# Optimization experiments

Hardware: AMD Instinct MI355X
Metric: run time of the kernel (lower is better)

## Reference

```python
import jax, jax.numpy as jnp
import numpy as np

B, N, C, H = 2, 2048, 1024, 16
D = C // H  # head dim = 64
EPS = 1e-12  # torch F.normalize eps


def l2norm(t):
    # F.normalize(t, dim=-1): x / max(||x||_2, eps)
    n = jnp.linalg.norm(t, axis=-1, keepdims=True)
    return t / jnp.maximum(n, EPS)


def setup_inputs() -> dict:
    key = jax.random.key(0)
    k1, k2, k3 = jax.random.split(key, 3)
    x = jax.random.normal(k1, (B, N, C), dtype=jnp.float32)
    qkv_w = jax.random.normal(k2, (3 * C, C), dtype=jnp.float32) * (1.0 / np.sqrt(C))
    temperature = jnp.ones((H, 1, 1), dtype=jnp.float32)
    proj_w = jax.random.normal(k3, (C, C), dtype=jnp.float32) * (1.0 / np.sqrt(C))
    proj_b = jnp.zeros((C,), dtype=jnp.float32)
    return {"x": x, "qkv_w": qkv_w, "temperature": temperature,
            "proj_w": proj_w, "proj_b": proj_b}


def reference(x, qkv_w, temperature, proj_w, proj_b):
    b, n, c = x.shape
    qkv = jnp.einsum('bnc,fc->bnf', x, qkv_w)           # [B,N,3C], no bias
    q, k, v = jnp.split(qkv, 3, axis=-1)                # each [B,N,C]
    # l2-normalize over FULL channel dim (before head split), as in source
    q = l2norm(q)
    k = l2norm(k)
    # split heads -> [B,H,N,D]
    q = q.reshape(b, n, H, D).transpose(0, 2, 1, 3)
    k = k.reshape(b, n, H, D).transpose(0, 2, 1, 3)
    v = v.reshape(b, n, H, D).transpose(0, 2, 1, 3)
    scale = 1.0 / np.sqrt(D)
    q = q * scale
    k = k * scale
    attn = jnp.einsum('bhnd,bhkd->bhnk', q, k)          # [B,H,N,N]
    attn = attn / temperature                           # (H,1,1) broadcasts
    attn = jax.nn.softmax(attn, axis=-1)
    out = jnp.einsum('bhnk,bhkd->bhnd', attn, v)        # [B,H,N,D]
    out = out.transpose(0, 2, 1, 3).reshape(b, n, c)    # [B,N,C]
    out = jnp.einsum('bnc,oc->bno', out, proj_w) + proj_b
    return out
```

## Files before the change

### kernel.cpp

```cpp
#include <hip/hip_runtime.h>

typedef __bf16 bf16;
using bf16x2 = __attribute__((ext_vector_type(2))) bf16;
using bf16x4 = __attribute__((ext_vector_type(4))) bf16;
using bf16x8 = __attribute__((ext_vector_type(8))) bf16;
using f32x4  = __attribute__((ext_vector_type(4))) float;

#define DEVI __device__ __forceinline__

DEVI void gload_lds16(const void* g, void* l) {
  __builtin_amdgcn_global_load_lds((const __attribute__((address_space(1))) void*)g,
                                   (__attribute__((address_space(3))) void*)l, 16, 0, 0);
}

DEVI float exp2_fast(float x) { return __builtin_amdgcn_exp2f(x); }

__global__ __launch_bounds__(256) void k_cvt3(
    const float* __restrict__ a, bf16* __restrict__ oa,
    const float* __restrict__ b, bf16* __restrict__ ob,
    const float* __restrict__ c, bf16* __restrict__ oc) {
  const int blk = blockIdx.x;
  const float* in; bf16* out; int i;
  if (blk < 4096)      { in = a; out = oa; i = blk * 256 + threadIdx.x; }
  else if (blk < 7168) { in = b; out = ob; i = (blk - 4096) * 256 + threadIdx.x; }
  else                 { in = c; out = oc; i = (blk - 7168) * 256 + threadIdx.x; }
  f32x4 v = ((const f32x4*)in)[i];
  bf16x4 o = {(bf16)v.x, (bf16)v.y, (bf16)v.z, (bf16)v.w};
  ((bf16x4*)out)[i] = o;
}

template<int OUT_BF16, int HAS_BIAS>
__global__ __launch_bounds__(256) void k_gemm_bt(
    const bf16* __restrict__ A, const bf16* __restrict__ W,
    const float* __restrict__ bias, void* __restrict__ outp,
    int Kk, int Nout)
{
  __shared__ __align__(16) bf16 As[128 * 32];
  __shared__ __align__(16) bf16 Bs[128 * 32];
  const int t = threadIdx.x;
  const int lane = t & 63, wv = t >> 6;
  const int l15 = lane & 15, l4 = lane >> 4;
  const int nbx = gridDim.x;
  const int fb = blockIdx.y * nbx + blockIdx.x;
  const int cpx = (nbx * gridDim.y) >> 3;
  const int swz = (fb & 7) * cpx + (fb >> 3);
  const int row0 = (swz % nbx) * 128, col0 = (swz / nbx) * 128;
  const int wr = wv >> 1, wc = wv & 1;

  f32x4 acc[4][4];
  #pragma unroll
  for (int m = 0; m < 4; ++m)
    #pragma unroll
    for (int n = 0; n < 4; ++n) acc[m][n] = (f32x4){0.f, 0.f, 0.f, 0.f};

  const int g0 = t, g1 = t + 256;
  const bf16* ga0 = A + (size_t)(row0 + (g0 >> 2)) * Kk + (g0 & 3) * 8;
  const bf16* ga1 = A + (size_t)(row0 + (g1 >> 2)) * Kk + (g1 & 3) * 8;
  const bf16* gb0 = W + (size_t)(col0 + (g0 >> 2)) * Kk + (g0 & 3) * 8;
  const bf16* gb1 = W + (size_t)(col0 + (g1 >> 2)) * Kk + (g1 & 3) * 8;
  char* la0 = (char*)As + wv * 1024;
  char* la1 = (char*)As + 4096 + wv * 1024;
  char* lb0 = (char*)Bs + wv * 1024;
  char* lb1 = (char*)Bs + 4096 + wv * 1024;

  const int nk = Kk >> 5;
  for (int kt = 0; kt < nk; ++kt) {
    __syncthreads();
    gload_lds16(ga0 + kt * 32, la0);
    gload_lds16(ga1 + kt * 32, la1);
    gload_lds16(gb0 + kt * 32, lb0);
    gload_lds16(gb1 + kt * 32, lb1);
    __syncthreads();
    bf16x8 af[4], bfv[4];
    #pragma unroll
    for (int m = 0; m < 4; ++m)
      af[m] = *(const bf16x8*)(As + (wr * 64 + m * 16 + l15) * 32 + l4 * 8);
    #pragma unroll
    for (int n = 0; n < 4; ++n)
      bfv[n] = *(const bf16x8*)(Bs + (wc * 64 + n * 16 + l15) * 32 + l4 * 8);
    #pragma unroll
    for (int m = 0; m < 4; ++m)
      #pragma unroll
      for (int n = 0; n < 4; ++n)
        acc[m][n] = __builtin_amdgcn_mfma_f32_16x16x32_bf16(af[m], bfv[n], acc[m][n], 0, 0, 0);
  }

  #pragma unroll
  for (int n = 0; n < 4; ++n) {
    const int col = col0 + wc * 64 + n * 16 + l15;
    float bv = HAS_BIAS ? bias[col] : 0.f;
    #pragma unroll
    for (int m = 0; m < 4; ++m) {
      #pragma unroll
      for (int r = 0; r < 4; ++r) {
        const int row = row0 + wr * 64 + m * 16 + l4 * 4 + r;
        float v = acc[m][n][r] + bv;
        if (OUT_BF16) ((bf16*)outp)[(size_t)row * Nout + col] = (bf16)v;
        else          ((float*)outp)[(size_t)row * Nout + col] = v;
      }
    }
  }
}

__global__ __launch_bounds__(256) void k_rownorm(const bf16* __restrict__ qkv,
                                                 float* __restrict__ invq,
                                                 float* __restrict__ invk)
{
  const int row = blockIdx.x * 4 + (threadIdx.x >> 6);
  const int lane = threadIdx.x & 63;
  const bf16* p = qkv + (size_t)row * 3072 + lane * 16;
  float sq = 0.f, sk = 0.f;
  bf16x8 a0 = *(const bf16x8*)(p);
  bf16x8 a1 = *(const bf16x8*)(p + 8);
  bf16x8 b0 = *(const bf16x8*)(p + 1024);
  bf16x8 b1 = *(const bf16x8*)(p + 1032);
  #pragma unroll
  for (int j = 0; j < 8; ++j) {
    float x0 = (float)a0[j], x1 = (float)a1[j];
    float y0 = (float)b0[j], y1 = (float)b1[j];
    sq += x0 * x0 + x1 * x1;
    sk += y0 * y0 + y1 * y1;
  }
  #pragma unroll
  for (int m = 1; m <= 32; m <<= 1) {
    sq += __shfl_xor(sq, m);
    sk += __shfl_xor(sk, m);
  }
  if (lane == 0) {
    invq[row] = 0.125f / fmaxf(sqrtf(sq), 1e-12f);
    invk[row] = 0.125f / fmaxf(sqrtf(sk), 1e-12f);
  }
}

__global__ __launch_bounds__(256) void k_scatter(
    const bf16* __restrict__ qkv, const float* __restrict__ invq,
    const float* __restrict__ invk, const float* __restrict__ temperature,
    bf16* __restrict__ Qh, bf16* __restrict__ Kh, bf16* __restrict__ Vt)
{
  __shared__ __align__(16) bf16 vt[64][72];
  const int t = threadIdx.x;
  const int b = blockIdx.z, h = blockIdx.y;
  const int n0 = blockIdx.x * 64;
  const float tfac = 1.4426950408889634f / temperature[h];
  {
    const int nl = t >> 2;
    const int d0 = (t & 3) << 4;
    const size_t row = (size_t)b * 2048 + n0 + nl;
    const bf16* src = qkv + row * 3072 + h * 64 + d0;
    const float fq = invq[row];
    const float fk = invk[row] * tfac;
    bf16x8 q0 = *(const bf16x8*)(src);
    bf16x8 q1 = *(const bf16x8*)(src + 8);
    bf16x8 k0 = *(const bf16x8*)(src + 1024);
    bf16x8 k1 = *(const bf16x8*)(src + 1032);
    bf16x8 v0 = *(const bf16x8*)(src + 2048);
    bf16x8 v1 = *(const bf16x8*)(src + 2056);
    bf16x8 qo, ko;
    #pragma unroll
    for (int j = 0; j < 8; ++j) {
      qo[j] = (bf16)((float)q0[j] * fq);
      ko[j] = (bf16)((float)k0[j] * fk);
    }
    size_t orow = ((size_t)(b * 16 + h) * 2048 + n0 + nl) * 64 + d0;
    *(bf16x8*)(Qh + orow) = qo;
    *(bf16x8*)(Kh + orow) = ko;
    #pragma unroll
    for (int j = 0; j < 8; ++j) {
      qo[j] = (bf16)((float)q1[j] * fq);
      ko[j] = (bf16)((float)k1[j] * fk);
    }
    *(bf16x8*)(Qh + orow + 8) = qo;
    *(bf16x8*)(Kh + orow + 8) = ko;
    *(bf16x8*)&vt[nl][d0] = v0;
    *(bf16x8*)&vt[nl][d0 + 8] = v1;
  }
  __syncthreads();
  {
    const int d = t >> 2;
    const int nc = (t & 3) << 4;
    bf16x8 o0, o1;
    #pragma unroll
    for (int j = 0; j < 8; ++j) { o0[j] = vt[nc + j][d]; o1[j] = vt[nc + 8 + j][d]; }
    size_t obase = ((size_t)(b * 16 + h) * 64 + d) * 2048 + n0 + nc;
    *(bf16x8*)(Vt + obase) = o0;
    *(bf16x8*)(Vt + obase + 8) = o1;
  }
}

__global__ __launch_bounds__(512, 4) void k_attn(
    const bf16* __restrict__ Qh, const bf16* __restrict__ Kh,
    const bf16* __restrict__ Vt, bf16* __restrict__ ao)
{
  __shared__ __align__(16) bf16 Kb[2][64 * 64];
  __shared__ __align__(16) bf16 Vb[2][64 * 64];
  __shared__ __align__(16) bf16 Pl[8][16 * 64];
  const int t = threadIdx.x, lane = t & 63, wv = t >> 6;
  const int l15 = lane & 15, l4 = lane >> 4;

  const int bid = blockIdx.x;
  const int swz = (bid & 7) * 64 + (bid >> 3);
  const int plane_id = swz >> 4;
  const int qb = swz & 15;
  const int b = plane_id >> 4, h = plane_id & 15;
  const int q0 = qb * 128 + wv * 16;

  const size_t plane = (size_t)plane_id * (2048 * 64);
  const bf16* Qp = Qh + plane;
  const bf16* Kp = Kh + plane;
  const bf16* Vp = Vt + plane;

  const int srow = t >> 3;
  const int sc = (t & 7) ^ (srow & 7);
  const bf16* gK = Kp + (size_t)srow * 64 + sc * 8;
  const bf16* gV = Vp + (size_t)srow * 2048 + sc * 8;
  char* lK0 = (char*)&Kb[0][0] + wv * 1024;
  char* lK1 = (char*)&Kb[1][0] + wv * 1024;
  char* lV0 = (char*)&Vb[0][0] + wv * 1024;
  char* lV1 = (char*)&Vb[1][0] + wv * 1024;

  bf16x8 qf0 = *(const bf16x8*)(Qp + (q0 + l15) * 64 + l4 * 8);
  bf16x8 qf1 = *(const bf16x8*)(Qp + (q0 + l15) * 64 + 32 + l4 * 8);

  bf16x8 vones;
  #pragma unroll
  for (int j = 0; j < 8; ++j) vones[j] = (bf16)1.0f;

  f32x4 accO[4];
  #pragma unroll
  for (int df = 0; df < 4; ++df) accO[df] = (f32x4){0.f, 0.f, 0.f, 0.f};
  f32x4 accS = (f32x4){0.f, 0.f, 0.f, 0.f};

  bf16* pw = &Pl[wv][0] + l15 * 64;
  const int pxor = (l15 & 7) << 3;

#define STAGE(bi, kv0_)                                           \
  do {                                                            \
    gload_lds16(gK + (size_t)(kv0_) * 64, (bi) ? lK1 : lK0);      \
    gload_lds16(gV + (kv0_),              (bi) ? lV1 : lV0);      \
  } while (0)

  STAGE(0, 0);
  __syncthreads();

  int cur = 0;
  for (int kt = 0; kt < 32; ++kt) {
    if (kt < 31) STAGE(cur ^ 1, (kt + 1) * 64);

    const bf16* kb = &Kb[cur][0];
    const bf16* vb = &Vb[cur][0];

    f32x4 s[4];
    __builtin_amdgcn_s_setprio(1);
    #pragma unroll
    for (int kvf = 0; kvf < 4; ++kvf) {
      const int row = kvf * 16 + l15;
      const int r7 = row & 7;
      bf16x8 kf0 = *(const bf16x8*)(kb + row * 64 + ((l4 ^ r7) * 8));
      bf16x8 kf1 = *(const bf16x8*)(kb + row * 64 + (((4 + l4) ^ r7) * 8));
      s[kvf] = (f32x4){0.f, 0.f, 0.f, 0.f};
      s[kvf] = __builtin_amdgcn_mfma_f32_16x16x32_bf16(kf0, qf0, s[kvf], 0, 0, 0);
      s[kvf] = __builtin_amdgcn_mfma_f32_16x16x32_bf16(kf1, qf1, s[kvf], 0, 0, 0);
    }
    __builtin_amdgcn_s_setprio(0);
    #pragma unroll
    for (int kvf = 0; kvf < 4; ++kvf)
      #pragma unroll
      for (int rp = 0; rp < 2; ++rp) {
        bf16x2 pv = {(bf16)exp2_fast(s[kvf][2 * rp]),
                     (bf16)exp2_fast(s[kvf][2 * rp + 1])};
        *(bf16x2*)(pw + ((kvf * 16 + l4 * 4 + 2 * rp) ^ pxor)) = pv;
      }
    __builtin_amdgcn_s_setprio(1);
    #pragma unroll
    for (int ss = 0; ss < 2; ++ss) {
      bf16x8 pf = *(const bf16x8*)(pw + (((ss * 32 + l4 * 8)) ^ pxor));
      accS = __builtin_amdgcn_mfma_f32_16x16x32_bf16(pf, vones, accS, 0, 0, 0);
      #pragma unroll
      for (int df = 0; df < 4; ++df) {
        const int row = df * 16 + l15;
        bf16x8 vf = *(const bf16x8*)(vb + row * 64 + (((ss * 4 + l4) ^ (row & 7)) * 8));
        accO[df] = __builtin_amdgcn_mfma_f32_16x16x32_bf16(pf, vf, accO[df], 0, 0, 0);
      }
    }
    __builtin_amdgcn_s_setprio(0);
    __syncthreads();
    cur ^= 1;
  }
#undef STAGE

  #pragma unroll
  for (int r = 0; r < 4; ++r) {
    const float inv = 1.f / accS[r];
    const size_t orow = ((size_t)b * 2048 + q0 + l4 * 4 + r) * 1024 + h * 64;
    #pragma unroll
    for (int df = 0; df < 4; ++df)
      ao[orow + df * 16 + l15] = (bf16)(accO[df][r] * inv);
  }
}

extern "C" void kernel_launch(void* const* d_in, const int* in_sizes, int n_in,
                              void* d_out, int out_size, void* d_ws, size_t ws_size,
                              hipStream_t stream)
{
  (void)in_sizes; (void)n_in; (void)out_size; (void)ws_size;
  const float* x      = (const float*)d_in[0];
  const float* qkv_w  = (const float*)d_in[1];
  const float* temp   = (const float*)d_in[2];
  const float* proj_w = (const float*)d_in[3];
  const float* proj_b = (const float*)d_in[4];
  float* out = (float*)d_out;

  char* w = (char*)d_ws;
  auto take = [&](size_t bytes) { char* p = w; w += (bytes + 255) & ~(size_t)255; return p; };
  bf16*  xb    = (bf16*)take((size_t)4096 * 1024 * 2);
  bf16*  wqkvb = (bf16*)take((size_t)3072 * 1024 * 2);
  bf16*  wpb   = (bf16*)take((size_t)1024 * 1024 * 2);
  bf16*  qkvb  = (bf16*)take((size_t)4096 * 3072 * 2);
  float* invq  = (float*)take((size_t)4096 * 4);
  float* invk  = (float*)take((size_t)4096 * 4);
  bf16*  Qh    = (bf16*)take((size_t)32 * 2048 * 64 * 2);
  bf16*  Kh    = (bf16*)take((size_t)32 * 2048 * 64 * 2);
  bf16*  Vt    = (bf16*)take((size_t)32 * 64 * 2048 * 2);
  bf16*  ao    = (bf16*)take((size_t)4096 * 1024 * 2);

  k_cvt3<<<8192, 256, 0, stream>>>(x, xb, qkv_w, wqkvb, proj_w, wpb);
  k_gemm_bt<1, 0><<<dim3(32, 24), 256, 0, stream>>>(xb, wqkvb, nullptr, qkvb, 1024, 3072);
  k_rownorm<<<1024, 256, 0, stream>>>(qkvb, invq, invk);
  k_scatter<<<dim3(32, 16, 2), 256, 0, stream>>>(qkvb, invq, invk, temp, Qh, Kh, Vt);
  k_attn<<<512, 512, 0, stream>>>(Qh, Kh, Vt, ao);
  k_gemm_bt<0, 1><<<dim3(32, 8), 256, 0, stream>>>(ao, wpb, proj_b, out, 1024, 1024);
}
```

Before: 203.0 us.

## Widen GEMM K-tile to 64 with XOR-swizzled LDS and fuse rownorm into scatter

The GEMM K-step per iteration doubles from 32 to 64. Global-to-LDS chunk placement uses an XOR swizzle on the row index so the wider rows do not cause LDS bank conflicts. This halves the number of sync barriers per GEMM and feeds twice as many MFMAs per tile load. Separately, the row-norm kernel is merged into the scatter kernel: each block computes norms for 64 rows into shared memory and then processes 4 heads. This removes a launch and the invq/invk round trip, but each block now recomputes norms redundantly (4x across blockIdx.y) and has fewer blocks in flight (256 instead of 1024).

```diff
diff --git a/kernel.cpp b/kernel.cpp
--- a/kernel.cpp
+++ b/kernel.cpp
@@ -35,8 +35,8 @@
     const float* __restrict__ bias, void* __restrict__ outp,
     int Kk, int Nout)
 {
-  __shared__ __align__(16) bf16 As[128 * 32];
-  __shared__ __align__(16) bf16 Bs[128 * 32];
+  __shared__ __align__(16) bf16 As[128 * 64];
+  __shared__ __align__(16) bf16 Bs[128 * 64];
   const int t = threadIdx.x;
   const int lane = t & 63, wv = t >> 6;
   const int l15 = lane & 15, l4 = lane >> 4;
@@ -53,36 +53,48 @@
     #pragma unroll
     for (int n = 0; n < 4; ++n) acc[m][n] = (f32x4){0.f, 0.f, 0.f, 0.f};
 
-  const int g0 = t, g1 = t + 256;
-  const bf16* ga0 = A + (size_t)(row0 + (g0 >> 2)) * Kk + (g0 & 3) * 8;
-  const bf16* ga1 = A + (size_t)(row0 + (g1 >> 2)) * Kk + (g1 & 3) * 8;
-  const bf16* gb0 = W + (size_t)(col0 + (g0 >> 2)) * Kk + (g0 & 3) * 8;
-  const bf16* gb1 = W + (size_t)(col0 + (g1 >> 2)) * Kk + (g1 & 3) * 8;
-  char* la0 = (char*)As + wv * 1024;
-  char* la1 = (char*)As + 4096 + wv * 1024;
-  char* lb0 = (char*)Bs + wv * 1024;
-  char* lb1 = (char*)Bs + 4096 + wv * 1024;
-
-  const int nk = Kk >> 5;
+  const bf16* gA[4];
+  const bf16* gB[4];
+  #pragma unroll
+  for (int j = 0; j < 4; ++j) {
+    const int c = t + j * 256;
+    const int row = c >> 3;
+    const int sc = (c & 7) ^ (row & 7);
+    gA[j] = A + (size_t)(row0 + row) * Kk + sc * 8;
+    gB[j] = W + (size_t)(col0 + row) * Kk + sc * 8;
+  }
+
+  const int nk = Kk >> 6;
   for (int kt = 0; kt < nk; ++kt) {
     __syncthreads();
-    gload_lds16(ga0 + kt * 32, la0);
-    gload_lds16(ga1 + kt * 32, la1);
-    gload_lds16(gb0 + kt * 32, lb0);
-    gload_lds16(gb1 + kt * 32, lb1);
-    __syncthreads();
-    bf16x8 af[4], bfv[4];
-    #pragma unroll
-    for (int m = 0; m < 4; ++m)
-      af[m] = *(const bf16x8*)(As + (wr * 64 + m * 16 + l15) * 32 + l4 * 8);
-    #pragma unroll
-    for (int n = 0; n < 4; ++n)
-      bfv[n] = *(const bf16x8*)(Bs + (wc * 64 + n * 16 + l15) * 32 + l4 * 8);
-    #pragma unroll
-    for (int m = 0; m < 4; ++m)
-      #pragma unroll
-      for (int n = 0; n < 4; ++n)
-        acc[m][n] = __builtin_amdgcn_mfma_f32_16x16x32_bf16(af[m], bfv[n], acc[m][n], 0, 0, 0);
+    #pragma unroll
+    for (int j = 0; j < 4; ++j) {
+      gload_lds16(gA[j] + kt * 64, (char*)As + wv * 1024 + j * 4096);
+      gload_lds16(gB[j] + kt * 64, (char*)Bs + wv * 1024 + j * 4096);
+    }
+    __syncthreads();
+    bf16x8 af[4][2], bfv[4][2];
+    #pragma unroll
+    for (int m = 0; m < 4; ++m) {
+      const int r = wr * 64 + m * 16 + l15;
+      const int r7 = r & 7;
+      af[m][0] = *(const bf16x8*)(As + r * 64 + ((l4 ^ r7) * 8));
+      af[m][1] = *(const bf16x8*)(As + r * 64 + (((4 + l4) ^ r7) * 8));
+    }
+    #pragma unroll
+    for (int n = 0; n < 4; ++n) {
+      const int r = wc * 64 + n * 16 + l15;
+      const int r7 = r & 7;
+      bfv[n][0] = *(const bf16x8*)(Bs + r * 64 + ((l4 ^ r7) * 8));
+      bfv[n][1] = *(const bf16x8*)(Bs + r * 64 + (((4 + l4) ^ r7) * 8));
+    }
+    #pragma unroll
+    for (int s = 0; s < 2; ++s)
+      #pragma unroll
+      for (int m = 0; m < 4; ++m)
+        #pragma unroll
+        for (int n = 0; n < 4; ++n)
+          acc[m][n] = __builtin_amdgcn_mfma_f32_16x16x32_bf16(af[m][s], bfv[n][s], acc[m][n], 0, 0, 0);
   }
 
   #pragma unroll
@@ -102,88 +114,89 @@
   }
 }
 
-__global__ __launch_bounds__(256) void k_rownorm(const bf16* __restrict__ qkv,
-                                                 float* __restrict__ invq,
-                                                 float* __restrict__ invk)
-{
-  const int row = blockIdx.x * 4 + (threadIdx.x >> 6);
-  const int lane = threadIdx.x & 63;
-  const bf16* p = qkv + (size_t)row * 3072 + lane * 16;
-  float sq = 0.f, sk = 0.f;
-  bf16x8 a0 = *(const bf16x8*)(p);
-  bf16x8 a1 = *(const bf16x8*)(p + 8);
-  bf16x8 b0 = *(const bf16x8*)(p + 1024);
-  bf16x8 b1 = *(const bf16x8*)(p + 1032);
-  #pragma unroll
-  for (int j = 0; j < 8; ++j) {
-    float x0 = (float)a0[j], x1 = (float)a1[j];
-    float y0 = (float)b0[j], y1 = (float)b1[j];
-    sq += x0 * x0 + x1 * x1;
-    sk += y0 * y0 + y1 * y1;
-  }
-  #pragma unroll
-  for (int m = 1; m <= 32; m <<= 1) {
-    sq += __shfl_xor(sq, m);
-    sk += __shfl_xor(sk, m);
-  }
-  if (lane == 0) {
-    invq[row] = 0.125f / fmaxf(sqrtf(sq), 1e-12f);
-    invk[row] = 0.125f / fmaxf(sqrtf(sk), 1e-12f);
-  }
-}
-
-__global__ __launch_bounds__(256) void k_scatter(
-    const bf16* __restrict__ qkv, const float* __restrict__ invq,
-    const float* __restrict__ invk, const float* __restrict__ temperature,
+__global__ __launch_bounds__(256) void k_normscatter(
+    const bf16* __restrict__ qkv, const float* __restrict__ temperature,
     bf16* __restrict__ Qh, bf16* __restrict__ Kh, bf16* __restrict__ Vt)
 {
+  __shared__ float invq_s[64], invk_s[64];
   __shared__ __align__(16) bf16 vt[64][72];
-  const int t = threadIdx.x;
-  const int b = blockIdx.z, h = blockIdx.y;
-  const int n0 = blockIdx.x * 64;
-  const float tfac = 1.4426950408889634f / temperature[h];
-  {
-    const int nl = t >> 2;
-    const int d0 = (t & 3) << 4;
-    const size_t row = (size_t)b * 2048 + n0 + nl;
-    const bf16* src = qkv + row * 3072 + h * 64 + d0;
-    const float fq = invq[row];
-    const float fk = invk[row] * tfac;
-    bf16x8 q0 = *(const bf16x8*)(src);
-    bf16x8 q1 = *(const bf16x8*)(src + 8);
-    bf16x8 k0 = *(const bf16x8*)(src + 1024);
-    bf16x8 k1 = *(const bf16x8*)(src + 1032);
-    bf16x8 v0 = *(const bf16x8*)(src + 2048);
-    bf16x8 v1 = *(const bf16x8*)(src + 2056);
-    bf16x8 qo, ko;
+  const int t = threadIdx.x, lane = t & 63, wv = t >> 6;
+  const int r0 = blockIdx.x * 64;
+  for (int rr = 0; rr < 16; ++rr) {
+    const int row = r0 + wv * 16 + rr;
+    const bf16* p = qkv + (size_t)row * 3072 + lane * 16;
+    float sq = 0.f, sk = 0.f;
+    bf16x8 a0 = *(const bf16x8*)(p);
+    bf16x8 a1 = *(const bf16x8*)(p + 8);
+    bf16x8 b0 = *(const bf16x8*)(p + 1024);
+    bf16x8 b1 = *(const bf16x8*)(p + 1032);
     #pragma unroll
     for (int j = 0; j < 8; ++j) {
-      qo[j] = (bf16)((float)q0[j] * fq);
-      ko[j] = (bf16)((float)k0[j] * fk);
-    }
-    size_t orow = ((size_t)(b * 16 + h) * 2048 + n0 + nl) * 64 + d0;
-    *(bf16x8*)(Qh + orow) = qo;
-    *(bf16x8*)(Kh + orow) = ko;
-    #pragma unroll
-    for (int j = 0; j < 8; ++j) {
-      qo[j] = (bf16)((float)q1[j] * fq);
-      ko[j] = (bf16)((float)k1[j] * fk);
-    }
-    *(bf16x8*)(Qh + orow + 8) = qo;
-    *(bf16x8*)(Kh + orow + 8) = ko;
-    *(bf16x8*)&vt[nl][d0] = v0;
-    *(bf16x8*)&vt[nl][d0 + 8] = v1;
+      float x0 = (float)a0[j], x1 = (float)a1[j];
+      float y0 = (float)b0[j], y1 = (float)b1[j];
+      sq += x0 * x0 + x1 * x1;
+      sk += y0 * y0 + y1 * y1;
+    }
+    #pragma unroll
+    for (int m = 1; m <= 32; m <<= 1) {
+      sq += __shfl_xor(sq, m);
+      sk += __shfl_xor(sk, m);
+    }
+    if (lane == 0) {
+      invq_s[wv * 16 + rr] = 0.125f / fmaxf(sqrtf(sq), 1e-12f);
+      invk_s[wv * 16 + rr] = 0.125f / fmaxf(sqrtf(sk), 1e-12f);
+    }
   }
   __syncthreads();
-  {
-    const int d = t >> 2;
-    const int nc = (t & 3) << 4;
-    bf16x8 o0, o1;
-    #pragma unroll
-    for (int j = 0; j < 8; ++j) { o0[j] = vt[nc + j][d]; o1[j] = vt[nc + 8 + j][d]; }
-    size_t obase = ((size_t)(b * 16 + h) * 64 + d) * 2048 + n0 + nc;
-    *(bf16x8*)(Vt + obase) = o0;
-    *(bf16x8*)(Vt + obase + 8) = o1;
+  const int b = r0 >> 11;
+  const int n0 = r0 & 2047;
+  const int nl = t >> 2;
+  const int d0 = (t & 3) << 4;
+  const int d = t >> 2;
+  const int nc = (t & 3) << 4;
+  for (int hi = 0; hi < 4; ++hi) {
+    const int h = blockIdx.y * 4 + hi;
+    const float tfac = 1.4426950408889634f / temperature[h];
+    {
+      const size_t row = (size_t)r0 + nl;
+      const bf16* src = qkv + row * 3072 + h * 64 + d0;
+      const float fq = invq_s[nl];
+      const float fk = invk_s[nl] * tfac;
+      bf16x8 q0 = *(const bf16x8*)(src);
+      bf16x8 q1 = *(const bf16x8*)(src + 8);
+      bf16x8 k0 = *(const bf16x8*)(src + 1024);
+      bf16x8 k1 = *(const bf16x8*)(src + 1032);
+      bf16x8 v0 = *(const bf16x8*)(src + 2048);
+      bf16x8 v1 = *(const bf16x8*)(src + 2056);
+      bf16x8 qo, ko;
+      #pragma unroll
+      for (int j = 0; j < 8; ++j) {
+        qo[j] = (bf16)((float)q0[j] * fq);
+        ko[j] = (bf16)((float)k0[j] * fk);
+      }
+      size_t orow = ((size_t)(b * 16 + h) * 2048 + n0 + nl) * 64 + d0;
+      *(bf16x8*)(Qh + orow) = qo;
+      *(bf16x8*)(Kh + orow) = ko;
+      #pragma unroll
+      for (int j = 0; j < 8; ++j) {
+        qo[j] = (bf16)((float)q1[j] * fq);
+        ko[j] = (bf16)((float)k1[j] * fk);
+      }
+      *(bf16x8*)(Qh + orow + 8) = qo;
+      *(bf16x8*)(Kh + orow + 8) = ko;
+      *(bf16x8*)&vt[nl][d0] = v0;
+      *(bf16x8*)&vt[nl][d0 + 8] = v1;
+    }
+    __syncthreads();
+    {
+      bf16x8 o0, o1;
+      #pragma unroll
+      for (int j = 0; j < 8; ++j) { o0[j] = vt[nc + j][d]; o1[j] = vt[nc + 8 + j][d]; }
+      size_t obase = ((size_t)(b * 16 + h) * 64 + d) * 2048 + n0 + nc;
+      *(bf16x8*)(Vt + obase) = o0;
+      *(bf16x8*)(Vt + obase + 8) = o1;
+    }
+    __syncthreads();
   }
 }
 
@@ -316,8 +329,6 @@
   bf16*  wqkvb = (bf16*)take((size_t)3072 * 1024 * 2);
   bf16*  wpb   = (bf16*)take((size_t)1024 * 1024 * 2);
   bf16*  qkvb  = (bf16*)take((size_t)4096 * 3072 * 2);
-  float* invq  = (float*)take((size_t)4096 * 4);
-  float* invk  = (float*)take((size_t)4096 * 4);
   bf16*  Qh    = (bf16*)take((size_t)32 * 2048 * 64 * 2);
   bf16*  Kh    = (bf16*)take((size_t)32 * 2048 * 64 * 2);
   bf16*  Vt    = (bf16*)take((size_t)32 * 64 * 2048 * 2);
@@ -325,8 +336,7 @@
 
   k_cvt3<<<8192, 256, 0, stream>>>(x, xb, qkv_w, wqkvb, proj_w, wpb);
   k_gemm_bt<1, 0><<<dim3(32, 24), 256, 0, stream>>>(xb, wqkvb, nullptr, qkvb, 1024, 3072);
-  k_rownorm<<<1024, 256, 0, stream>>>(qkvb, invq, invk);
-  k_scatter<<<dim3(32, 16, 2), 256, 0, stream>>>(qkvb, invq, invk, temp, Qh, Kh, Vt);
+  k_normscatter<<<dim3(64, 4), 256, 0, stream>>>(qkvb, temp, Qh, Kh, Vt);
   k_attn<<<512, 512, 0, stream>>>(Qh, Kh, Vt, ao);
   k_gemm_bt<0, 1><<<dim3(32, 8), 256, 0, stream>>>(ao, wpb, proj_b, out, 1024, 1024);
 }
```

Measured after the change: 202.2 us. Within noise of the previous version (-0.4%).
